# Performance work log

Measured on AMD Instinct MI355X. Metric: run time of the kernel, lower is better.

The kernel has to match this reference:

```python
import jax, jax.numpy as jnp
import numpy as np

N_NODES = 50000
N_EDGES = 800000
IN_F = 128
OUT_F = 64


def setup_inputs() -> dict:
    key = jax.random.key(0)
    k1, k2, k3, k4, k5, k6 = jax.random.split(key, 6)
    x = jax.random.normal(k1, (N_NODES, IN_F), dtype=jnp.float32)
    edge_src = jax.random.randint(k2, (N_EDGES,), 0, N_NODES, dtype=jnp.int32)
    edge_dst = jax.random.randint(k3, (N_EDGES,), 0, N_NODES, dtype=jnp.int32)
    # normalized adjacency values (e.g. D^-1/2 A D^-1/2 entries) -> small positive floats
    edge_weight = jax.random.uniform(k4, (N_EDGES,), dtype=jnp.float32)
    std_v = 1.0 / np.sqrt(OUT_F)
    weight = jax.random.uniform(k5, (IN_F, OUT_F), dtype=jnp.float32, minval=-std_v, maxval=std_v)
    bias = jax.random.uniform(k6, (OUT_F,), dtype=jnp.float32, minval=-std_v, maxval=std_v)
    return {"x": x, "edge_src": edge_src, "edge_dst": edge_dst,
            "edge_weight": edge_weight, "weight": weight, "bias": bias}


def reference(x, edge_src, edge_dst, edge_weight, weight, bias):
    # support = x @ W  : [N, out]
    support = jnp.matmul(x, weight)
    # spmm(adj, support) with adj in COO form: out[d] = sum_e w_e * support[s_e]
    msgs = edge_weight[:, None] * support[edge_src]  # [E, out]
    agg = jax.ops.segment_sum(msgs, edge_dst, num_segments=N_NODES)  # [N, out]
    return agg + bias
```

## Files before the change

kernel.cpp:

```cpp
#include <hip/hip_runtime.h>
#include <hip/hip_bf16.h>

#define IN_F 128
#define OUT_F 64
#define NXCD 8
#define CAP 64
#define XST 136

typedef __attribute__((ext_vector_type(8))) short short8;
typedef __attribute__((ext_vector_type(4))) short short4v;
typedef __attribute__((ext_vector_type(4))) float f32x4;

__device__ inline unsigned short f2bf(float f) {
    unsigned u = __float_as_uint(f);
    return (unsigned short)((u + 0x7FFF + ((u >> 16) & 1)) >> 16);
}

__global__ __launch_bounds__(256) void gcn_matmul_mfma(
    const float* __restrict__ x, const float* __restrict__ w,
    __hip_bfloat16* __restrict__ support, int n_nodes,
    int* __restrict__ counts)
{
    __shared__ short xbf[64 * XST];
    __shared__ short wt [64 * XST];

    const int tid  = threadIdx.x;
    const int row0 = blockIdx.x * 64;

    for (int i = blockIdx.x * 256 + tid; i < n_nodes; i += gridDim.x * 256)
        counts[i] = 0;

    const float4* x4 = (const float4*)x;
    for (int i = tid; i < 64 * 32; i += 256) {
        int r = i >> 5, k4 = i & 31;
        int gr = row0 + r;
        float4 v = (gr < n_nodes) ? x4[(size_t)gr * 32 + k4]
                                  : make_float4(0.f, 0.f, 0.f, 0.f);
        short4v sv;
        sv.x = (short)f2bf(v.x); sv.y = (short)f2bf(v.y);
        sv.z = (short)f2bf(v.z); sv.w = (short)f2bf(v.w);
        *(short4v*)&xbf[r * XST + k4 * 4] = sv;
    }
    for (int i = tid; i < IN_F * OUT_F; i += 256) {
        int k = i >> 6, c = i & 63;
        wt[c * XST + k] = (short)f2bf(w[i]);
    }
    __syncthreads();

    const int lane = tid & 63;
    const int wv   = tid >> 6;
    const int lm   = lane & 15;
    const int lg   = lane >> 4;

    short8 af[4];
    const short* abase = &xbf[(wv * 16 + lm) * XST + lg * 8];
    #pragma unroll
    for (int ks = 0; ks < 4; ++ks)
        af[ks] = *(const short8*)(abase + ks * 32);

    f32x4 acc[4];
    #pragma unroll
    for (int j0 = 0; j0 < 4; ++j0) { acc[j0].x = acc[j0].y = acc[j0].z = acc[j0].w = 0.f; }

    #pragma unroll
    for (int j0 = 0; j0 < 4; ++j0) {
        const short* bbase = &wt[(j0 * 16 + lm) * XST + lg * 8];
        #pragma unroll
        for (int ks = 0; ks < 4; ++ks) {
            short8 bf = *(const short8*)(bbase + ks * 32);
            acc[j0] = __builtin_amdgcn_mfma_f32_16x16x32_bf16(af[ks], bf, acc[j0], 0, 0, 0);
        }
    }

    #pragma unroll
    for (int j0 = 0; j0 < 4; ++j0) {
        int col = j0 * 16 + lm;
        #pragma unroll
        for (int r = 0; r < 4; ++r) {
            int row = row0 + wv * 16 + lg * 4 + r;
            if (row < n_nodes)
                support[(size_t)row * OUT_F + col] = __float2bfloat16(acc[j0][r]);
        }
    }
}

__global__ __launch_bounds__(256) void gcn_bucket(
    const int4* __restrict__ edst4, const int4* __restrict__ esrc4,
    const float4* __restrict__ ewgt4, int* __restrict__ counts,
    unsigned* __restrict__ pairs, int n_edges4, int n_edges,
    int n_nodes, int stride4)
{
    int g = blockIdx.x & (NXCD - 1);
    int j = blockIdx.x >> 3;
    int chunk = (n_nodes + NXCD - 1) / NXCD;
    int lo = g * chunk;
    int hi = lo + chunk; if (hi > n_nodes) hi = n_nodes;

    #pragma unroll 2
    for (int e4 = j * 256 + threadIdx.x; e4 < n_edges4; e4 += stride4) {
        int4   d4 = edst4[e4];
        int4   s4 = esrc4[e4];
        float4 w4 = ewgt4[e4];
        #pragma unroll
        for (int t = 0; t < 4; ++t) {
            int d = (&d4.x)[t];
            if (d >= lo && d < hi) {
                unsigned p = ((unsigned)(&s4.x)[t] << 16) | f2bf((&w4.x)[t]);
                int pos = atomicAdd(&counts[d], 1);
                if (pos < CAP)
                    pairs[(size_t)d * CAP + pos] = p;
            }
        }
    }
    if (j == 0) {
        const int*   esrc = (const int*)esrc4;
        const int*   edst = (const int*)edst4;
        const float* ewgt = (const float*)ewgt4;
        for (int e = n_edges4 * 4 + threadIdx.x; e < n_edges; e += 256) {
            int d = edst[e];
            if (d >= lo && d < hi) {
                unsigned p = ((unsigned)esrc[e] << 16) | f2bf(ewgt[e]);
                int pos = atomicAdd(&counts[d], 1);
                if (pos < CAP)
                    pairs[(size_t)d * CAP + pos] = p;
            }
        }
    }
}

__global__ __launch_bounds__(256) void gcn_gather(
    const __hip_bfloat16* __restrict__ support, const int* __restrict__ counts,
    const unsigned* __restrict__ pairs, const float* __restrict__ bias,
    float* __restrict__ out, int n_nodes)
{
    int wid = (blockIdx.x * 256 + threadIdx.x) >> 6;
    if (wid >= n_nodes) return;
    int lane = threadIdx.x & 63;

    int deg = counts[wid]; if (deg > CAP) deg = CAP;

    unsigned p = 0;
    if (lane < deg) p = pairs[(size_t)wid * CAP + lane];
    int   my_s = (int)(p >> 16);
    float my_w = __uint_as_float((p & 0xFFFFu) << 16);

    float acc = 0.0f;
    int d = 0;
    for (; d + 4 <= deg; d += 4) {
        int   s0 = __shfl(my_s, d),     s1 = __shfl(my_s, d + 1);
        int   s2 = __shfl(my_s, d + 2), s3 = __shfl(my_s, d + 3);
        float w0 = __shfl(my_w, d),     w1 = __shfl(my_w, d + 1);
        float w2 = __shfl(my_w, d + 2), w3 = __shfl(my_w, d + 3);
        float v0 = __bfloat162float(support[(size_t)s0 * OUT_F + lane]);
        float v1 = __bfloat162float(support[(size_t)s1 * OUT_F + lane]);
        float v2 = __bfloat162float(support[(size_t)s2 * OUT_F + lane]);
        float v3 = __bfloat162float(support[(size_t)s3 * OUT_F + lane]);
        acc = fmaf(w0, v0, acc);
        acc = fmaf(w1, v1, acc);
        acc = fmaf(w2, v2, acc);
        acc = fmaf(w3, v3, acc);
    }
    for (; d < deg; ++d) {
        int   s = __shfl(my_s, d);
        float w = __shfl(my_w, d);
        acc = fmaf(w, __bfloat162float(support[(size_t)s * OUT_F + lane]), acc);
    }
    out[wid * OUT_F + lane] = acc + bias[lane];
}

extern "C" void kernel_launch(void* const* d_in, const int* in_sizes, int n_in,
                              void* d_out, int out_size, void* d_ws, size_t ws_size,
                              hipStream_t stream) {
    const float* x    = (const float*)d_in[0];
    const int*   esrc = (const int*)d_in[1];
    const int*   edst = (const int*)d_in[2];
    const float* ewgt = (const float*)d_in[3];
    const float* w    = (const float*)d_in[4];
    const float* bias = (const float*)d_in[5];
    float* out = (float*)d_out;

    const int n_nodes = in_sizes[0] / IN_F;
    const int n_edges = in_sizes[1];

    char* ws = (char*)d_ws;
    size_t sup_bytes = (((size_t)n_nodes * OUT_F * sizeof(__hip_bfloat16)) + 15) & ~15ull;
    size_t cnt_bytes = (((size_t)n_nodes * sizeof(int)) + 15) & ~15ull;

    __hip_bfloat16* support = (__hip_bfloat16*)ws;   ws += sup_bytes;
    int*      counts = (int*)ws;                     ws += cnt_bytes;
    unsigned* pairs  = (unsigned*)ws;

    int mm_blocks = (n_nodes + 63) / 64;
    gcn_matmul_mfma<<<mm_blocks, 256, 0, stream>>>(x, w, support, n_nodes, counts);

    const int BPG = 256;
    int n_edges4 = n_edges / 4;
    gcn_bucket<<<NXCD * BPG, 256, 0, stream>>>(
        (const int4*)edst, (const int4*)esrc, (const float4*)ewgt,
        counts, pairs, n_edges4, n_edges, n_nodes, BPG * 256);

    int gb = (n_nodes + 3) / 4;
    gcn_gather<<<gb, 256, 0, stream>>>(support, counts, pairs, bias, out, n_nodes);
}
```

Baseline: 82.91 us.

## Pre-partition edges into per-XCD queues before atomic placement

Replaces the bucket kernel, where every XCD group reads all edges and keeps only its own destination range, with two passes. A binscan pass reads each edge once and sorts it into 8 destination-range bins in shared memory, then flushes them to global per-group queues. A place pass then has each group read only its own queue and do the counts atomics and pair stores. This cuts the 8x redundant edge reads but adds a kernel launch, a queue write and read round trip, and packs dst and src into 16 bits each, which assumes fewer than 65536 nodes.

```diff
diff --git a/kernel.cpp b/kernel.cpp
--- a/kernel.cpp
+++ b/kernel.cpp
@@ -6,6 +6,7 @@
 #define NXCD 8
 #define CAP 64
 #define XST 136
+#define BINCAP 512
 
 typedef __attribute__((ext_vector_type(8))) short short8;
 typedef __attribute__((ext_vector_type(4))) short short4v;
@@ -19,7 +20,7 @@
 __global__ __launch_bounds__(256) void gcn_matmul_mfma(
     const float* __restrict__ x, const float* __restrict__ w,
     __hip_bfloat16* __restrict__ support, int n_nodes,
-    int* __restrict__ counts)
+    int* __restrict__ counts, int zero_ints)
 {
     __shared__ short xbf[64 * XST];
     __shared__ short wt [64 * XST];
@@ -27,7 +28,7 @@
     const int tid  = threadIdx.x;
     const int row0 = blockIdx.x * 64;
 
-    for (int i = blockIdx.x * 256 + tid; i < n_nodes; i += gridDim.x * 256)
+    for (int i = blockIdx.x * 256 + tid; i < zero_ints; i += gridDim.x * 256)
         counts[i] = 0;
 
     const float4* x4 = (const float4*)x;
@@ -84,6 +85,71 @@
     }
 }
 
+__global__ __launch_bounds__(256) void gcn_binscan(
+    const int* __restrict__ edst, const int* __restrict__ esrc,
+    const float* __restrict__ ewgt, int* __restrict__ qcur,
+    int2* __restrict__ queue, int n_edges, int n_nodes, int qseg)
+{
+    __shared__ int2 bins[NXCD][BINCAP];
+    __shared__ int  bincnt[NXCD];
+
+    const int tid = threadIdx.x;
+    if (tid < NXCD) bincnt[tid] = 0;
+    __syncthreads();
+
+    int per   = (n_edges + gridDim.x - 1) / gridDim.x;
+    int start = blockIdx.x * per;
+    int end   = start + per; if (end > n_edges) end = n_edges;
+
+    for (int e = start + tid; e < end; e += 256) {
+        int   d = edst[e];
+        int   s = esrc[e];
+        float w = ewgt[e];
+        int g = (int)(((unsigned)d * NXCD) / (unsigned)n_nodes);
+        int2 rec = make_int2((d << 16) | s, __float_as_int(w));
+        int lidx = atomicAdd(&bincnt[g], 1);
+        if (lidx < BINCAP) {
+            bins[g][lidx] = rec;
+        } else {
+            int gp = atomicAdd(&qcur[g], 1);
+            queue[(size_t)g * qseg + gp] = rec;
+        }
+    }
+    __syncthreads();
+
+    const int lane = tid & 63;
+    const int wv   = tid >> 6;
+    for (int bin = wv; bin < NXCD; bin += 4) {
+        int cnt = bincnt[bin]; if (cnt > BINCAP) cnt = BINCAP;
+        int base = 0;
+        if (lane == 0) base = atomicAdd(&qcur[bin], cnt);
+        base = __shfl(base, 0);
+        for (int i = lane; i < cnt; i += 64)
+            queue[(size_t)bin * qseg + base + i] = bins[bin][i];
+    }
+}
+
+__global__ __launch_bounds__(256) void gcn_place(
+    const int2* __restrict__ queue, const int* __restrict__ qcur,
+    int* __restrict__ counts, unsigned* __restrict__ pairs, int qseg)
+{
+    int g = blockIdx.x & (NXCD - 1);
+    int j = blockIdx.x >> 3;
+    int qlen = qcur[g];
+    const int2* q = &queue[(size_t)g * qseg];
+    int stride = (gridDim.x >> 3) * 256;
+
+    for (int i = j * 256 + threadIdx.x; i < qlen; i += stride) {
+        int2 rec = q[i];
+        int d = (unsigned)rec.x >> 16;
+        int s = rec.x & 0xFFFF;
+        unsigned p = ((unsigned)s << 16) | f2bf(__int_as_float(rec.y));
+        int pos = atomicAdd(&counts[d], 1);
+        if (pos < CAP)
+            pairs[(size_t)d * CAP + pos] = p;
+    }
+}
+
 __global__ __launch_bounds__(256) void gcn_bucket(
     const int4* __restrict__ edst4, const int4* __restrict__ esrc4,
     const float4* __restrict__ ewgt4, int* __restrict__ counts,
@@ -96,7 +162,6 @@
     int lo = g * chunk;
     int hi = lo + chunk; if (hi > n_nodes) hi = n_nodes;
 
-    #pragma unroll 2
     for (int e4 = j * 256 + threadIdx.x; e4 < n_edges4; e4 += stride4) {
         int4   d4 = edst4[e4];
         int4   s4 = esrc4[e4];
@@ -183,21 +248,39 @@
     const int n_edges = in_sizes[1];
 
     char* ws = (char*)d_ws;
-    size_t sup_bytes = (((size_t)n_nodes * OUT_F * sizeof(__hip_bfloat16)) + 15) & ~15ull;
-    size_t cnt_bytes = (((size_t)n_nodes * sizeof(int)) + 15) & ~15ull;
+    size_t sup_bytes  = (((size_t)n_nodes * OUT_F * sizeof(__hip_bfloat16)) + 15) & ~15ull;
+    size_t cnt_bytes  = (((size_t)n_nodes * sizeof(int)) + 15) & ~15ull;
+    size_t qcur_bytes = 16 * sizeof(int);
+    size_t pair_bytes = (size_t)n_nodes * CAP * sizeof(unsigned);
 
     __hip_bfloat16* support = (__hip_bfloat16*)ws;   ws += sup_bytes;
     int*      counts = (int*)ws;                     ws += cnt_bytes;
-    unsigned* pairs  = (unsigned*)ws;
+    int*      qcur   = (int*)ws;                     ws += qcur_bytes;
+    unsigned* pairs  = (unsigned*)ws;                ws += pair_bytes;
+    int2*     queue  = (int2*)ws;
+
+    int qseg = n_edges / NXCD + 8192;
+    size_t need = sup_bytes + cnt_bytes + qcur_bytes + pair_bytes
+                + (size_t)NXCD * qseg * sizeof(int2);
+
+    int zero_ints = (int)((cnt_bytes + qcur_bytes) / sizeof(int));
 
     int mm_blocks = (n_nodes + 63) / 64;
-    gcn_matmul_mfma<<<mm_blocks, 256, 0, stream>>>(x, w, support, n_nodes, counts);
-
-    const int BPG = 256;
-    int n_edges4 = n_edges / 4;
-    gcn_bucket<<<NXCD * BPG, 256, 0, stream>>>(
-        (const int4*)edst, (const int4*)esrc, (const float4*)ewgt,
-        counts, pairs, n_edges4, n_edges, n_nodes, BPG * 256);
+    gcn_matmul_mfma<<<mm_blocks, 256, 0, stream>>>(x, w, support, n_nodes,
+                                                   counts, zero_ints);
+
+    if (need <= ws_size) {
+        gcn_binscan<<<256, 256, 0, stream>>>(edst, esrc, ewgt, qcur, queue,
+                                             n_edges, n_nodes, qseg);
+        const int BPG2 = 256;
+        gcn_place<<<NXCD * BPG2, 256, 0, stream>>>(queue, qcur, counts, pairs, qseg);
+    } else {
+        const int BPG = 256;
+        int n_edges4 = n_edges / 4;
+        gcn_bucket<<<NXCD * BPG, 256, 0, stream>>>(
+            (const int4*)edst, (const int4*)esrc, (const float4*)ewgt,
+            counts, pairs, n_edges4, n_edges, n_nodes, BPG * 256);
+    }
 
     int gb = (n_nodes + 3) / 4;
     gcn_gather<<<gb, 256, 0, stream>>>(support, counts, pairs, bias, out, n_nodes);
```

Result: slower. 109.2 us (+31.8%).

## Fuse matmul and edge bucketing into one interleaved kernel with separate zeroing

Applied to the files above, without the earlier changes.

Merges the MFMA matmul and the edge-bucketing pass into a single launch: every fourth row of blocks computes a 64-row support tile and the rest bucket edges, so the compute-bound and atomic-bound work run concurrently on the GPU. Because the two halves now run at the same time, counts zeroing moves into its own small kernel that runs first. The matmul path also loads x straight from global memory into MFMA registers instead of staging it through LDS. The cost is a third launch for zeroing, and the bucket path uses a different grid size and stride than the tuned version it replaces.

```diff
diff --git a/kernel.cpp b/kernel.cpp
--- a/kernel.cpp
+++ b/kernel.cpp
@@ -5,10 +5,9 @@
 #define OUT_F 64
 #define NXCD 8
 #define CAP 64
-#define XST 136
+#define WST 136
 
 typedef __attribute__((ext_vector_type(8))) short short8;
-typedef __attribute__((ext_vector_type(4))) short short4v;
 typedef __attribute__((ext_vector_type(4))) float f32x4;
 
 __device__ inline unsigned short f2bf(float f) {
@@ -16,113 +15,123 @@
     return (unsigned short)((u + 0x7FFF + ((u >> 16) & 1)) >> 16);
 }
 
-__global__ __launch_bounds__(256) void gcn_matmul_mfma(
+__global__ __launch_bounds__(256) void gcn_zero(int4* __restrict__ p, int n4)
+{
+    int stride = gridDim.x * 256;
+    for (int i = blockIdx.x * 256 + threadIdx.x; i < n4; i += stride)
+        p[i] = make_int4(0, 0, 0, 0);
+}
+
+__global__ __launch_bounds__(256) void gcn_fused(
     const float* __restrict__ x, const float* __restrict__ w,
-    __hip_bfloat16* __restrict__ support, int n_nodes,
-    int* __restrict__ counts)
+    __hip_bfloat16* __restrict__ support,
+    const int4* __restrict__ edst4, const int4* __restrict__ esrc4,
+    const float4* __restrict__ ewgt4,
+    int* __restrict__ counts, unsigned* __restrict__ pairs,
+    int n_nodes, int n_edges4, int n_edges,
+    int mm_tiles, int bstride)
 {
-    __shared__ short xbf[64 * XST];
-    __shared__ short wt [64 * XST];
-
-    const int tid  = threadIdx.x;
-    const int row0 = blockIdx.x * 64;
-
-    for (int i = blockIdx.x * 256 + tid; i < n_nodes; i += gridDim.x * 256)
-        counts[i] = 0;
-
-    const float4* x4 = (const float4*)x;
-    for (int i = tid; i < 64 * 32; i += 256) {
-        int r = i >> 5, k4 = i & 31;
-        int gr = row0 + r;
-        float4 v = (gr < n_nodes) ? x4[(size_t)gr * 32 + k4]
-                                  : make_float4(0.f, 0.f, 0.f, 0.f);
-        short4v sv;
-        sv.x = (short)f2bf(v.x); sv.y = (short)f2bf(v.y);
-        sv.z = (short)f2bf(v.z); sv.w = (short)f2bf(v.w);
-        *(short4v*)&xbf[r * XST + k4 * 4] = sv;
-    }
-    for (int i = tid; i < IN_F * OUT_F; i += 256) {
-        int k = i >> 6, c = i & 63;
-        wt[c * XST + k] = (short)f2bf(w[i]);
-    }
-    __syncthreads();
-
-    const int lane = tid & 63;
-    const int wv   = tid >> 6;
-    const int lm   = lane & 15;
-    const int lg   = lane >> 4;
-
-    short8 af[4];
-    const short* abase = &xbf[(wv * 16 + lm) * XST + lg * 8];
-    #pragma unroll
-    for (int ks = 0; ks < 4; ++ks)
-        af[ks] = *(const short8*)(abase + ks * 32);
-
-    f32x4 acc[4];
-    #pragma unroll
-    for (int j0 = 0; j0 < 4; ++j0) { acc[j0].x = acc[j0].y = acc[j0].z = acc[j0].w = 0.f; }
-
-    #pragma unroll
-    for (int j0 = 0; j0 < 4; ++j0) {
-        const short* bbase = &wt[(j0 * 16 + lm) * XST + lg * 8];
+    __shared__ short wt[64 * WST];
+
+    const int tid = threadIdx.x;
+    const int q   = blockIdx.x >> 3;
+    const int r   = blockIdx.x & 7;
+
+    if ((q & 3) == 3) {
+        int tile = (q >> 2) * 8 + r;
+        if (tile >= mm_tiles) return;
+        int row0 = tile * 64;
+
+        for (int i = tid; i < IN_F * OUT_F; i += 256) {
+            int k = i >> 6, c = i & 63;
+            wt[c * WST + k] = (short)f2bf(w[i]);
+        }
+        __syncthreads();
+
+        const int lane = tid & 63;
+        const int wv   = tid >> 6;
+        const int lm   = lane & 15;
+        const int lg   = lane >> 4;
+
+        int gr = row0 + wv * 16 + lm;
+        bool rok = (gr < n_nodes);
+        const float4* x4 = (const float4*)x;
+        size_t xb = (size_t)gr * 32;
+
+        short8 af[4];
         #pragma unroll
         for (int ks = 0; ks < 4; ++ks) {
-            short8 bf = *(const short8*)(bbase + ks * 32);
-            acc[j0] = __builtin_amdgcn_mfma_f32_16x16x32_bf16(af[ks], bf, acc[j0], 0, 0, 0);
-        }
-    }
-
-    #pragma unroll
-    for (int j0 = 0; j0 < 4; ++j0) {
-        int col = j0 * 16 + lm;
-        #pragma unroll
-        for (int r = 0; r < 4; ++r) {
-            int row = row0 + wv * 16 + lg * 4 + r;
-            if (row < n_nodes)
-                support[(size_t)row * OUT_F + col] = __float2bfloat16(acc[j0][r]);
-        }
-    }
-}
-
-__global__ __launch_bounds__(256) void gcn_bucket(
-    const int4* __restrict__ edst4, const int4* __restrict__ esrc4,
-    const float4* __restrict__ ewgt4, int* __restrict__ counts,
-    unsigned* __restrict__ pairs, int n_edges4, int n_edges,
-    int n_nodes, int stride4)
-{
-    int g = blockIdx.x & (NXCD - 1);
-    int j = blockIdx.x >> 3;
-    int chunk = (n_nodes + NXCD - 1) / NXCD;
-    int lo = g * chunk;
-    int hi = lo + chunk; if (hi > n_nodes) hi = n_nodes;
-
-    #pragma unroll 2
-    for (int e4 = j * 256 + threadIdx.x; e4 < n_edges4; e4 += stride4) {
-        int4   d4 = edst4[e4];
-        int4   s4 = esrc4[e4];
-        float4 w4 = ewgt4[e4];
-        #pragma unroll
-        for (int t = 0; t < 4; ++t) {
-            int d = (&d4.x)[t];
-            if (d >= lo && d < hi) {
-                unsigned p = ((unsigned)(&s4.x)[t] << 16) | f2bf((&w4.x)[t]);
-                int pos = atomicAdd(&counts[d], 1);
-                if (pos < CAP)
-                    pairs[(size_t)d * CAP + pos] = p;
-            }
-        }
-    }
-    if (j == 0) {
-        const int*   esrc = (const int*)esrc4;
-        const int*   edst = (const int*)edst4;
-        const float* ewgt = (const float*)ewgt4;
-        for (int e = n_edges4 * 4 + threadIdx.x; e < n_edges; e += 256) {
-            int d = edst[e];
-            if (d >= lo && d < hi) {
-                unsigned p = ((unsigned)esrc[e] << 16) | f2bf(ewgt[e]);
-                int pos = atomicAdd(&counts[d], 1);
-                if (pos < CAP)
-                    pairs[(size_t)d * CAP + pos] = p;
+            float4 a = rok ? x4[xb + ks * 8 + lg * 2]
+                           : make_float4(0.f, 0.f, 0.f, 0.f);
+            float4 b = rok ? x4[xb + ks * 8 + lg * 2 + 1]
+                           : make_float4(0.f, 0.f, 0.f, 0.f);
+            short8 v;
+            v[0] = (short)f2bf(a.x); v[1] = (short)f2bf(a.y);
+            v[2] = (short)f2bf(a.z); v[3] = (short)f2bf(a.w);
+            v[4] = (short)f2bf(b.x); v[5] = (short)f2bf(b.y);
+            v[6] = (short)f2bf(b.z); v[7] = (short)f2bf(b.w);
+            af[ks] = v;
+        }
+
+        f32x4 acc[4];
+        #pragma unroll
+        for (int j0 = 0; j0 < 4; ++j0)
+            { acc[j0].x = acc[j0].y = acc[j0].z = acc[j0].w = 0.f; }
+
+        #pragma unroll
+        for (int j0 = 0; j0 < 4; ++j0) {
+            const short* bbase = &wt[(j0 * 16 + lm) * WST + lg * 8];
+            #pragma unroll
+            for (int ks = 0; ks < 4; ++ks) {
+                short8 bf = *(const short8*)(bbase + ks * 32);
+                acc[j0] = __builtin_amdgcn_mfma_f32_16x16x32_bf16(af[ks], bf, acc[j0], 0, 0, 0);
+            }
+        }
+
+        #pragma unroll
+        for (int j0 = 0; j0 < 4; ++j0) {
+            int col = j0 * 16 + lm;
+            #pragma unroll
+            for (int rr = 0; rr < 4; ++rr) {
+                int row = row0 + wv * 16 + lg * 4 + rr;
+                if (row < n_nodes)
+                    support[(size_t)row * OUT_F + col] = __float2bfloat16(acc[j0][rr]);
+            }
+        }
+    } else {
+        int g  = r;
+        int jb = q - (q >> 2);
+        int chunk = (n_nodes + NXCD - 1) / NXCD;
+        int lo = g * chunk;
+        int hi = lo + chunk; if (hi > n_nodes) hi = n_nodes;
+
+        for (int e4 = jb * 256 + tid; e4 < n_edges4; e4 += bstride) {
+            int4   d4 = edst4[e4];
+            int4   s4 = esrc4[e4];
+            float4 w4 = ewgt4[e4];
+            #pragma unroll
+            for (int t = 0; t < 4; ++t) {
+                int d = (&d4.x)[t];
+                if (d >= lo && d < hi) {
+                    unsigned p = ((unsigned)(&s4.x)[t] << 16) | f2bf((&w4.x)[t]);
+                    int pos = atomicAdd(&counts[d], 1);
+                    if (pos < CAP)
+                        pairs[(size_t)d * CAP + pos] = p;
+                }
+            }
+        }
+        if (jb == 0) {
+            const int*   esrc = (const int*)esrc4;
+            const int*   edst = (const int*)edst4;
+            const float* ewgt = (const float*)ewgt4;
+            for (int e = n_edges4 * 4 + tid; e < n_edges; e += 256) {
+                int d = edst[e];
+                if (d >= lo && d < hi) {
+                    unsigned p = ((unsigned)esrc[e] << 16) | f2bf(ewgt[e]);
+                    int pos = atomicAdd(&counts[d], 1);
+                    if (pos < CAP)
+                        pairs[(size_t)d * CAP + pos] = p;
+                }
             }
         }
     }
@@ -190,14 +199,17 @@
     int*      counts = (int*)ws;                     ws += cnt_bytes;
     unsigned* pairs  = (unsigned*)ws;
 
-    int mm_blocks = (n_nodes + 63) / 64;
-    gcn_matmul_mfma<<<mm_blocks, 256, 0, stream>>>(x, w, support, n_nodes, counts);
-
-    const int BPG = 256;
+    gcn_zero<<<64, 256, 0, stream>>>((int4*)counts, (int)(cnt_bytes / 16));
+
+    int mm_tiles = (n_nodes + 63) / 64;
+    int msr = (mm_tiles + 7) / 8;
+    int total_sr = msr * 4;
+    int bucket_rows = total_sr - msr;
+    int bstride = bucket_rows * 256;
     int n_edges4 = n_edges / 4;
-    gcn_bucket<<<NXCD * BPG, 256, 0, stream>>>(
-        (const int4*)edst, (const int4*)esrc, (const float4*)ewgt,
-        counts, pairs, n_edges4, n_edges, n_nodes, BPG * 256);
+    gcn_fused<<<total_sr * 8, 256, 0, stream>>>(
+        x, w, support, (const int4*)edst, (const int4*)esrc, (const float4*)ewgt,
+        counts, pairs, n_nodes, n_edges4, n_edges, mm_tiles, bstride);
 
     int gb = (n_nodes + 3) / 4;
     gcn_gather<<<gb, 256, 0, stream>>>(support, counts, pairs, bias, out, n_nodes);
```

New measurement: 77.77 us. 6.2% less time.
